# Kernel tuning notes

Hardware: AMD Instinct MI355X
Metric: run time of the kernel (lower is better)

Reference implementation:

```python
import jax, jax.numpy as jnp
import numpy as np

B, T, E, H = 2, 1024, 2048, 32
D = E // H
GROUP = (0.25, 0.25, 0.25, 0.25)
NEG = float(np.finfo(np.float32).min)


def quant_per_token(t, n_bits):
    # smoothquant-style: clamp(absmax, 1e-5) / qmax, per last-dim row
    qmax = 2 ** (n_bits - 1) - 1
    s = jnp.clip(jnp.abs(t).max(-1, keepdims=True), 1e-5, None) / qmax
    return jnp.round(t / s) * s


def w8a8_linear(x, W, b, quant_out=False):
    xq = quant_per_token(x, 8)           # per-token act quant
    Wq = quant_per_token(W, 8)           # per-output-channel weight quant (W: [out, in])
    y = xq @ Wq.T + b
    return quant_per_token(y, 8) if quant_out else y


def to_heads(x):
    # [B, T, E] -> [B*H, T, D]
    return x.reshape(B, T, H, D).transpose(0, 2, 1, 3).reshape(B * H, T, D)


def setup_inputs() -> dict:
    key = jax.random.key(0)
    ks = jax.random.split(key, 9)
    hidden_states = jax.random.normal(ks[0], (B, T, E), jnp.float32)
    causal = jnp.where(jnp.tril(jnp.ones((T, T), bool)), 0.0, NEG).astype(jnp.float32)
    attention_mask = jnp.broadcast_to(causal[None, None], (B, 1, T, T))
    w = 0.02
    return {
        'hidden_states': hidden_states,
        'attention_mask': attention_mask,
        'Wq': jax.random.normal(ks[1], (E, E), jnp.float32) * w,
        'bq': jax.random.normal(ks[2], (E,), jnp.float32) * w,
        'Wk': jax.random.normal(ks[3], (E, E), jnp.float32) * w,
        'bk': jax.random.normal(ks[4], (E,), jnp.float32) * w,
        'Wv': jax.random.normal(ks[5], (E, E), jnp.float32) * w,
        'bv': jax.random.normal(ks[6], (E,), jnp.float32) * w,
        'Wo': jax.random.normal(ks[7], (E, E), jnp.float32) * w,
        'bo': jax.random.normal(ks[8], (E,), jnp.float32) * w,
    }


def reference(hidden_states, attention_mask, Wq, bq, Wk, bk, Wv, bv, Wo, bo):
    scaling = D ** -0.5
    q = w8a8_linear(hidden_states, Wq, bq, quant_out=True) * scaling  # [B,T,E]
    k = w8a8_linear(hidden_states, Wk, bk)                            # [B,T,E]
    v = w8a8_linear(hidden_states, Wv, bv)                            # [B,T,E]

    # ---- heavy-hitter scoring pass (pre-4bit-quant K) ----
    q1, k1 = to_heads(q), to_heads(k)                                 # [BH,T,D]
    aw = jnp.einsum('btd,bsd->bts', q1, k1)                           # [BH,T,T]
    aw = aw.reshape(B, H, T, T) + attention_mask
    aw = jnp.maximum(aw, NEG).reshape(B * H, T, T)
    tmp_attn = jax.nn.softmax(aw, axis=-1)
    acc = tmp_attn.sum(axis=1).sum(axis=0)[None, :]                   # [1,T]
    row_vector = jnp.arange(T, 0, -1).astype(jnp.float32)[None, :]    # T, T-1, ..., 1
    acc = acc / row_vector / (B * H)

    # ---- group-wise top-k heavy-hitter selection ----
    range_size_or = int(T / len(GROUP) / 2)
    start = 1
    idx_list = []
    for i, ratio in enumerate(GROUP):
        rs = int(T * ratio)
        end = min(start + rs - 1, T) if i < len(GROUP) - 1 else T
        partial = acc[:, start - 1:end]
        _, ti = jax.lax.top_k(partial, range_size_or)
        idx_list.append(ti + start - 1)
        start = end + 1
    topk_idx = jnp.concatenate(idx_list, axis=-1).reshape(-1)

    # ---- mixed-precision K quantization ----
    k_abs = jnp.abs(k)
    # fake_quant_mix (8-bit): amax(...)[0] in torch indexes batch 0 -> scales [T,1]
    s_mix = jnp.clip(k_abs.max(-1, keepdims=True)[0] / 127.0, 1e-5, None)  # [T,1]
    k_imp = jnp.round(k / s_mix) * s_mix
    # fake_quant (4-bit, per-row): clamp then divide by 7
    s4 = jnp.clip(k_abs.max(-1, keepdims=True), 1e-5, None) / 7.0
    kq = jnp.round(k / s4) * s4
    kq = kq.at[:, topk_idx, :].set(k_imp[:, topk_idx, :])
    # fake_quant_v (4-bit, per-tensor)
    sv = jnp.clip(jnp.abs(v).max(), 1e-5, None) / 7.0
    vq = jnp.round(v / sv) * sv

    # ---- actual attention with quantized K/V ----
    q2, k2, v2 = to_heads(q), to_heads(kq), to_heads(vq)
    aw2 = jnp.einsum('btd,bsd->bts', q2, k2).reshape(B, H, T, T) + attention_mask
    aw2 = jnp.maximum(aw2, NEG).reshape(B * H, T, T)
    probs = jax.nn.softmax(aw2, axis=-1)
    out = jnp.einsum('bts,bsd->btd', probs, v2)                       # [BH,T,D]
    out = out.reshape(B, H, T, D).transpose(0, 2, 1, 3).reshape(B, T, E)
    return w8a8_linear(out, Wo, bo)
```

## Files before the change

### kernel.cpp

```cpp
#include <hip/hip_runtime.h>
#include <stdint.h>

#define NEG_INF (-__builtin_inff())
#define L2E 1.4426950408889634f

namespace {
constexpr int kT   = 1024;
constexpr int kE   = 2048;
}

using bf16x8 = __attribute__((ext_vector_type(8))) short;
using f32x4  = __attribute__((ext_vector_type(4))) float;
using i32x4  = __attribute__((ext_vector_type(4))) int;

#define MFMA_BF16(a, b, c) __builtin_amdgcn_mfma_f32_16x16x32_bf16((a), (b), (c), 0, 0, 0)
#define MFMA_I8(a, b, c)   __builtin_amdgcn_mfma_i32_16x16x64_i8((a), (b), (c), 0, 0, 0)

__device__ __forceinline__ void gload16(const void* g, void* l) {
  __builtin_amdgcn_global_load_lds((const __attribute__((address_space(1))) unsigned*)g,
                                   (__attribute__((address_space(3))) unsigned*)l, 16, 0, 0);
}
__device__ __forceinline__ unsigned bfr(float x) {
  unsigned u = __float_as_uint(x);
  return (u + 0x7FFFu + ((u >> 16) & 1u)) >> 16;
}
__device__ __forceinline__ float bf2f(unsigned h) { return __uint_as_float(h << 16); }
__device__ __forceinline__ unsigned pk2(float a, float b) { return bfr(a) | (bfr(b) << 16); }
__device__ __forceinline__ float fexp2(float x) { return __builtin_amdgcn_exp2f(x); }

__device__ __forceinline__ float waveReduceMax(float v) {
#pragma unroll
  for (int o = 32; o > 0; o >>= 1) v = fmaxf(v, __shfl_down(v, o, 64));
  return v;
}
__device__ __forceinline__ float waveReduceSum(float v) {
#pragma unroll
  for (int o = 32; o > 0; o >>= 1) v += __shfl_down(v, o, 64);
  return v;
}
__device__ __forceinline__ float blockMax256(float v, float* r4) {
  const int tid = threadIdx.x;
  float wm = waveReduceMax(v);
  if ((tid & 63) == 0) r4[tid >> 6] = wm;
  __syncthreads();
  float bm = fmaxf(fmaxf(r4[0], r4[1]), fmaxf(r4[2], r4[3]));
  __syncthreads();
  return bm;
}

__global__ __launch_bounds__(256) void k_rowquant_i8(const float* __restrict__ X,
                                                     int8_t* __restrict__ Xq,
                                                     float* __restrict__ S) {
  const int row = blockIdx.x;
  const int tid = threadIdx.x;
  const float* x = X + (size_t)row * kE;
  __shared__ float r4[4];
  float am = 0.f;
#pragma unroll
  for (int it = 0; it < 2; ++it) {
    const float4 v = *reinterpret_cast<const float4*>(x + (size_t)(it * 256 + tid) * 4);
    am = fmaxf(am, fmaxf(fmaxf(fabsf(v.x), fabsf(v.y)), fmaxf(fabsf(v.z), fabsf(v.w))));
  }
  const float bm = blockMax256(am, r4);
  const float s = fmaxf(bm, 1e-5f) / 127.f;
  int8_t* xq = Xq + (size_t)row * kE;
#pragma unroll
  for (int it = 0; it < 2; ++it) {
    const int i = (it * 256 + tid) * 4;
    const float4 v = *reinterpret_cast<const float4*>(x + i);
    char4 q;
    q.x = (char)(int)rintf(v.x / s);
    q.y = (char)(int)rintf(v.y / s);
    q.z = (char)(int)rintf(v.z / s);
    q.w = (char)(int)rintf(v.w / s);
    *reinterpret_cast<char4*>(xq + i) = q;
  }
  if (tid == 0) S[row] = s;
}

__global__ __launch_bounds__(256) void k_rowquant_w4(const float* __restrict__ W0,
                                                     const float* __restrict__ W1,
                                                     const float* __restrict__ W2,
                                                     const float* __restrict__ W3,
                                                     int8_t* __restrict__ Q0,
                                                     int8_t* __restrict__ Q1,
                                                     int8_t* __restrict__ Q2,
                                                     int8_t* __restrict__ Q3,
                                                     float* __restrict__ S) {
  const int y = blockIdx.y;
  const float* W = (y == 0) ? W0 : (y == 1) ? W1 : (y == 2) ? W2 : W3;
  int8_t* Qp = (y == 0) ? Q0 : (y == 1) ? Q1 : (y == 2) ? Q2 : Q3;
  const int row = blockIdx.x;
  const int tid = threadIdx.x;
  const float* x = W + (size_t)row * kE;
  __shared__ float r4[4];
  float am = 0.f;
#pragma unroll
  for (int it = 0; it < 2; ++it) {
    const float4 v = *reinterpret_cast<const float4*>(x + (size_t)(it * 256 + tid) * 4);
    am = fmaxf(am, fmaxf(fmaxf(fabsf(v.x), fabsf(v.y)), fmaxf(fabsf(v.z), fabsf(v.w))));
  }
  const float bm = blockMax256(am, r4);
  const float s = fmaxf(bm, 1e-5f) / 127.f;
  int8_t* xq = Qp + (size_t)row * kE;
#pragma unroll
  for (int it = 0; it < 2; ++it) {
    const int i = (it * 256 + tid) * 4;
    const float4 v = *reinterpret_cast<const float4*>(x + i);
    char4 q;
    q.x = (char)(int)rintf(v.x / s);
    q.y = (char)(int)rintf(v.y / s);
    q.z = (char)(int)rintf(v.z / s);
    q.w = (char)(int)rintf(v.w / s);
    *reinterpret_cast<char4*>(xq + i) = q;
  }
  if (tid == 0) S[y * kE + row] = s;
}

__global__ __launch_bounds__(256) void k_q2int(const float* __restrict__ Qb,
                                               short* __restrict__ qi,
                                               float* __restrict__ sqg) {
  const int row = blockIdx.x;
  const int tid = threadIdx.x;
  const float* x = Qb + (size_t)row * kE;
  __shared__ float r4[4];
  float am = 0.f;
  float4 v[2];
#pragma unroll
  for (int it = 0; it < 2; ++it) {
    v[it] = *reinterpret_cast<const float4*>(x + (size_t)(it * 256 + tid) * 4);
    am = fmaxf(am, fmaxf(fmaxf(fabsf(v[it].x), fabsf(v[it].y)), fmaxf(fabsf(v[it].z), fabsf(v[it].w))));
  }
  const float bm = blockMax256(am, r4);
  const float s = fmaxf(bm, 1e-5f) / 127.f;
#pragma unroll
  for (int it = 0; it < 2; ++it) {
    const int i = (it * 256 + tid) * 4;
    short4 q;
    q.x = (short)bfr(rintf(v[it].x / s));
    q.y = (short)bfr(rintf(v[it].y / s));
    q.z = (short)bfr(rintf(v[it].z / s));
    q.w = (short)bfr(rintf(v[it].w / s));
    *reinterpret_cast<short4*>(qi + (size_t)row * kE + i) = q;
  }
  if (tid == 0) sqg[row] = s * 0.125f;
}

__global__ __launch_bounds__(256) void k_ksplitscale(const float* __restrict__ Kb,
                                                     short* __restrict__ khi,
                                                     short* __restrict__ klo,
                                                     float* __restrict__ s4,
                                                     float* __restrict__ smix) {
  const int row = blockIdx.x;
  const int tid = threadIdx.x;
  const float* x = Kb + (size_t)row * kE;
  __shared__ float r4[4];
  float am = 0.f;
  float4 v[2];
#pragma unroll
  for (int it = 0; it < 2; ++it) {
    v[it] = *reinterpret_cast<const float4*>(x + (size_t)(it * 256 + tid) * 4);
    am = fmaxf(am, fmaxf(fmaxf(fabsf(v[it].x), fabsf(v[it].y)), fmaxf(fabsf(v[it].z), fabsf(v[it].w))));
  }
  const float bm = blockMax256(am, r4);
#pragma unroll
  for (int it = 0; it < 2; ++it) {
    const int i = (it * 256 + tid) * 4;
    short4 hh, ll;
    unsigned hb;
    hb = bfr(v[it].x); hh.x = (short)hb; ll.x = (short)bfr(v[it].x - bf2f(hb));
    hb = bfr(v[it].y); hh.y = (short)hb; ll.y = (short)bfr(v[it].y - bf2f(hb));
    hb = bfr(v[it].z); hh.z = (short)hb; ll.z = (short)bfr(v[it].z - bf2f(hb));
    hb = bfr(v[it].w); hh.w = (short)hb; ll.w = (short)bfr(v[it].w - bf2f(hb));
    *reinterpret_cast<short4*>(khi + (size_t)row * kE + i) = hh;
    *reinterpret_cast<short4*>(klo + (size_t)row * kE + i) = ll;
  }
  if (tid == 0) {
    s4[row] = fmaxf(bm, 1e-5f) / 7.f;
    if (row < kT) smix[row] = fmaxf(bm / 127.f, 1e-5f);
  }
}

__global__ void k_init(unsigned* vmax) {
  if (threadIdx.x == 0 && blockIdx.x == 0) *vmax = 0u;
}

__global__ __launch_bounds__(256) void k_vabsmax(const float* __restrict__ Vb,
                                                 unsigned* __restrict__ vmax) {
  const int row = blockIdx.x;
  const int tid = threadIdx.x;
  const float* x = Vb + (size_t)row * kE;
  __shared__ float r4[4];
  float am = 0.f;
#pragma unroll
  for (int it = 0; it < 2; ++it) {
    const float4 v = *reinterpret_cast<const float4*>(x + (size_t)(it * 256 + tid) * 4);
    am = fmaxf(am, fmaxf(fmaxf(fabsf(v.x), fabsf(v.y)), fmaxf(fabsf(v.z), fabsf(v.w))));
  }
  const float bm = blockMax256(am, r4);
  if (tid == 0) atomicMax(vmax, __float_as_uint(bm));
}

__global__ __launch_bounds__(256) void k_kint(const float* __restrict__ Kb,
                                              const float* __restrict__ s4,
                                              const float* __restrict__ smix,
                                              const int* __restrict__ sel,
                                              short* __restrict__ ki,
                                              float* __restrict__ skg) {
  const int row = blockIdx.x;
  const int tid = threadIdx.x;
  const int t = row & (kT - 1);
  const float s = sel[t] ? smix[t] : s4[row];
  const float* x = Kb + (size_t)row * kE;
#pragma unroll
  for (int it = 0; it < 2; ++it) {
    const int i = (it * 256 + tid) * 4;
    const float4 v = *reinterpret_cast<const float4*>(x + i);
    short4 q;
    q.x = (short)bfr(rintf(v.x / s));
    q.y = (short)bfr(rintf(v.y / s));
    q.z = (short)bfr(rintf(v.z / s));
    q.w = (short)bfr(rintf(v.w / s));
    *reinterpret_cast<short4*>(ki + (size_t)row * kE + i) = q;
  }
  if (tid == 0) skg[row] = s;
}

__global__ __launch_bounds__(256) void k_vint(const float* __restrict__ Vb,
                                              const unsigned* __restrict__ vmax,
                                              short* __restrict__ vt) {
  const int tt = blockIdx.x;
  const int bh = blockIdx.y;
  const int b = bh >> 5, h = bh & 31;
  const float sv = fmaxf(__uint_as_float(*vmax), 1e-5f) / 7.f;
  __shared__ short tr[64][80];
  const int tid = threadIdx.x;
#pragma unroll
  for (int i = 0; i < 4; ++i) {
    const int e = i * 256 + tid;
    const int tok = e >> 4, d4 = (e & 15) * 4;
    const float4 v = *reinterpret_cast<const float4*>(
        &Vb[(size_t)(b * kT + tt * 64 + tok) * kE + h * 64 + d4]);
    tr[d4 + 0][tok] = (short)bfr(rintf(v.x / sv));
    tr[d4 + 1][tok] = (short)bfr(rintf(v.y / sv));
    tr[d4 + 2][tok] = (short)bfr(rintf(v.z / sv));
    tr[d4 + 3][tok] = (short)bfr(rintf(v.w / sv));
  }
  __syncthreads();
#pragma unroll
  for (int i = 0; i < 2; ++i) {
    const int e = i * 256 + tid;
    const int d = e >> 3, u = e & 7;
    const bf16x8 row = *reinterpret_cast<const bf16x8*>(&tr[d][u * 8]);
    *reinterpret_cast<bf16x8*>(&vt[(size_t)(bh * 64 + d) * kT + tt * 64 + u * 8]) = row;
  }
}

__device__ __forceinline__ void gemm_i8_body(const int8_t* __restrict__ A,
                                             const float* __restrict__ sa,
                                             const int8_t* __restrict__ Bw,
                                             const float* __restrict__ sw,
                                             const float* __restrict__ bias,
                                             float* __restrict__ Y,
                                             int8_t* As0, int8_t* As1,
                                             int8_t* Bs0, int8_t* Bs1) {
  int8_t* Asb[2] = {As0, As1};
  int8_t* Bsb[2] = {Bs0, Bs1};
  const int tid = threadIdx.x;
  const int lane = tid & 63, w = tid >> 6;
  const int g = lane >> 4, c16 = lane & 15;
  const int m0 = blockIdx.y * 128, n0 = blockIdx.x * 128;
  const int wm = (w >> 1) * 64, wn = (w & 1) * 64;

  const i32x4 zero = {0, 0, 0, 0};
  i32x4 acc[4][4];
#pragma unroll
  for (int i = 0; i < 4; ++i)
#pragma unroll
    for (int j = 0; j < 4; ++j) acc[i][j] = zero;

  const int srow = tid >> 2, su = tid & 3;
  auto stage = [&](int buf, int k0) {
#pragma unroll
    for (int i = 0; i < 2; ++i) {
      const int row = i * 64 + srow;
      const int uoff = ((su ^ (row & 3)) << 4);
      gload16(A + (size_t)(m0 + row) * kE + k0 + uoff, &Asb[buf][row * 64 + su * 16]);
      gload16(Bw + (size_t)(n0 + row) * kE + k0 + uoff, &Bsb[buf][row * 64 + su * 16]);
    }
  };

  stage(0, 0);
  __syncthreads();
  int cur = 0;
  for (int k0 = 0; k0 < kE; k0 += 64) {
    if (k0 + 64 < kE) stage(cur ^ 1, k0 + 64);
    i32x4 av[4], bv[4];
#pragma unroll
    for (int f = 0; f < 4; ++f) {
      const int ar = wm + f * 16 + c16;
      av[f] = *reinterpret_cast<const i32x4*>(&Asb[cur][ar * 64 + ((g ^ (c16 & 3)) << 4)]);
      const int br = wn + f * 16 + c16;
      bv[f] = *reinterpret_cast<const i32x4*>(&Bsb[cur][br * 64 + ((g ^ (c16 & 3)) << 4)]);
    }
#pragma unroll
    for (int fm = 0; fm < 4; ++fm)
#pragma unroll
      for (int fn = 0; fn < 4; ++fn) acc[fm][fn] = MFMA_I8(av[fm], bv[fn], acc[fm][fn]);
    __syncthreads();
    cur ^= 1;
  }

#pragma unroll
  for (int fn = 0; fn < 4; ++fn) {
    const int n = n0 + wn + fn * 16 + c16;
    const float swn = sw[n], bn = bias[n];
#pragma unroll
    for (int fm = 0; fm < 4; ++fm) {
#pragma unroll
      for (int r = 0; r < 4; ++r) {
        const int m = m0 + wm + fm * 16 + g * 4 + r;
        Y[(size_t)m * kE + n] = (float)acc[fm][fn][r] * sa[m] * swn + bn;
      }
    }
  }
}

__global__ __launch_bounds__(256) void k_gemm_i8(const int8_t* __restrict__ A,
                                                 const float* __restrict__ sa,
                                                 const int8_t* __restrict__ Bw,
                                                 const float* __restrict__ sw,
                                                 const float* __restrict__ bias,
                                                 float* __restrict__ Y) {
  __shared__ int8_t As[2][128 * 64];
  __shared__ int8_t Bs[2][128 * 64];
  gemm_i8_body(A, sa, Bw, sw, bias, Y, As[0], As[1], Bs[0], Bs[1]);
}

__global__ __launch_bounds__(256) void k_gemm_qkv(const int8_t* __restrict__ A,
                                                  const float* __restrict__ sa,
                                                  const int8_t* __restrict__ Wq,
                                                  const int8_t* __restrict__ Wk,
                                                  const int8_t* __restrict__ Wv,
                                                  const float* __restrict__ sWall,
                                                  const float* __restrict__ bq,
                                                  const float* __restrict__ bk,
                                                  const float* __restrict__ bv,
                                                  float* __restrict__ qb,
                                                  float* __restrict__ kb,
                                                  float* __restrict__ vb) {
  __shared__ int8_t As[2][128 * 64];
  __shared__ int8_t Bs[2][128 * 64];
  const int z = blockIdx.z;
  const int8_t* Bw = (z == 0) ? Wq : (z == 1) ? Wk : Wv;
  const float* sw = sWall + (size_t)z * kE;
  const float* bias = (z == 0) ? bq : (z == 1) ? bk : bv;
  float* Y = (z == 0) ? qb : (z == 1) ? kb : vb;
  gemm_i8_body(A, sa, Bw, sw, bias, Y, As[0], As[1], Bs[0], Bs[1]);
}

__global__ __launch_bounds__(256) void k_attn1(const short* __restrict__ qi,
                                               const short* __restrict__ khi,
                                               const short* __restrict__ klo,
                                               const float* __restrict__ sqg,
                                               float* __restrict__ accPart) {
  const int r1 = blockIdx.x, r2 = 15 - r1, bh = blockIdx.y;
  const int b = bh >> 5, h = bh & 31;
  const int tid = threadIdx.x, lane = tid & 63, w = tid >> 6;
  const int g = lane >> 4, c16 = lane & 15;
  const int swz = c16 & 7;

  __shared__ short qs1[64 * 64];
  __shared__ short qs2[64 * 64];
  __shared__ short hbuf[2][64 * 64];
  __shared__ short lbuf[2][64 * 64];
  __shared__ float accL[1024];
  __shared__ float Arow[128], Crow[128];

  for (int i = tid; i < 1024; i += 256) accL[i] = 0.f;

  const int st8 = tid >> 3, su = tid & 7;
  {
    const int tokb1 = b * kT + r1 * 64;
    const int tokb2 = b * kT + r2 * 64;
#pragma unroll
    for (int i = 0; i < 2; ++i) {
      const int tok = i * 32 + st8;
      const int co = ((su ^ (tok & 7)) << 3);
      gload16(qi + (size_t)(tokb1 + tok) * kE + h * 64 + co, &qs1[tok * 64 + su * 8]);
      gload16(qi + (size_t)(tokb2 + tok) * kE + h * 64 + co, &qs2[tok * 64 + su * 8]);
    }
  }
  auto stage = [&](int buf, int kt) {
    const int tokb = b * kT + kt * 64;
#pragma unroll
    for (int i = 0; i < 2; ++i) {
      const int tok = i * 32 + st8;
      const size_t gsrc = (size_t)(tokb + tok) * kE + h * 64 + ((su ^ (tok & 7)) << 3);
      gload16(khi + gsrc, &hbuf[buf][tok * 64 + su * 8]);
      gload16(klo + gsrc, &lbuf[buf][tok * 64 + su * 8]);
    }
  };

  stage(0, 0);
  __syncthreads();

  const int qrow = w * 16 + c16;
  const bf16x8 q1_0 = *reinterpret_cast<const bf16x8*>(&qs1[qrow * 64 + ((g ^ swz) << 3)]);
  const bf16x8 q1_1 = *reinterpret_cast<const bf16x8*>(&qs1[qrow * 64 + (((4 + g) ^ swz) << 3)]);
  const bf16x8 q2_0 = *reinterpret_cast<const bf16x8*>(&qs2[qrow * 64 + ((g ^ swz) << 3)]);
  const bf16x8 q2_1 = *reinterpret_cast<const bf16x8*>(&qs2[qrow * 64 + (((4 + g) ^ swz) << 3)]);
  const float A1c = sqg[b * kT + r1 * 64 + qrow] * L2E;
  const float A2c = sqg[b * kT + r2 * 64 + qrow] * L2E;

  float m1 = NEG_INF, l1 = 0.f, m2_ = NEG_INF, l2 = 0.f;
  int cur = 0;

  for (int kt = 0; kt <= r2; ++kt) {
    if (kt < r2) stage(cur ^ 1, kt + 1);
    const bool act1 = kt <= r1;
    float p1[4][4], p2[4][4];
    float pm1 = NEG_INF, pm2 = NEG_INF;
#pragma unroll
    for (int f = 0; f < 4; ++f) {
      const int tokl = f * 16 + c16;
      const bf16x8 ah0 = *reinterpret_cast<const bf16x8*>(&hbuf[cur][tokl * 64 + ((g ^ swz) << 3)]);
      const bf16x8 ah1 = *reinterpret_cast<const bf16x8*>(&hbuf[cur][tokl * 64 + (((4 + g) ^ swz) << 3)]);
      const bf16x8 al0 = *reinterpret_cast<const bf16x8*>(&lbuf[cur][tokl * 64 + ((g ^ swz) << 3)]);
      const bf16x8 al1 = *reinterpret_cast<const bf16x8*>(&lbuf[cur][tokl * 64 + (((4 + g) ^ swz) << 3)]);
      f32x4 sB = {0.f, 0.f, 0.f, 0.f};
      sB = MFMA_BF16(ah0, q2_0, sB);
      sB = MFMA_BF16(ah1, q2_1, sB);
      sB = MFMA_BF16(al0, q2_0, sB);
      sB = MFMA_BF16(al1, q2_1, sB);
      f32x4 sA = {0.f, 0.f, 0.f, 0.f};
      if (act1) {
        sA = MFMA_BF16(ah0, q1_0, sA);
        sA = MFMA_BF16(ah1, q1_1, sA);
        sA = MFMA_BF16(al0, q1_0, sA);
        sA = MFMA_BF16(al1, q1_1, sA);
      }
#pragma unroll
      for (int r = 0; r < 4; ++r) {
        const int tokd = f * 16 + g * 4 + r;
        float s2 = sB[r] * A2c;
        if (kt == r2 && tokd > qrow) s2 = NEG_INF;
        p2[f][r] = s2;
        pm2 = fmaxf(pm2, s2);
        float s1 = sA[r] * A1c;
        if (kt == r1 && tokd > qrow) s1 = NEG_INF;
        p1[f][r] = s1;
        pm1 = fmaxf(pm1, s1);
      }
    }
    {
      pm2 = fmaxf(pm2, __shfl_xor(pm2, 16));
      pm2 = fmaxf(pm2, __shfl_xor(pm2, 32));
      const bool upd = pm2 > m2_ + 8.f;
      const float mn = upd ? fmaxf(m2_, pm2) : m2_;
      const float fsc = fexp2(m2_ - mn);
      float rs = 0.f;
#pragma unroll
      for (int f = 0; f < 4; ++f)
#pragma unroll
        for (int r = 0; r < 4; ++r) rs += fexp2(p2[f][r] - mn);
      rs += __shfl_xor(rs, 16);
      rs += __shfl_xor(rs, 32);
      l2 = l2 * fsc + rs;
      m2_ = mn;
    }
    if (act1) {
      pm1 = fmaxf(pm1, __shfl_xor(pm1, 16));
      pm1 = fmaxf(pm1, __shfl_xor(pm1, 32));
      const bool upd = pm1 > m1 + 8.f;
      const float mn = upd ? fmaxf(m1, pm1) : m1;
      const float fsc = fexp2(m1 - mn);
      float rs = 0.f;
#pragma unroll
      for (int f = 0; f < 4; ++f)
#pragma unroll
        for (int r = 0; r < 4; ++r) rs += fexp2(p1[f][r] - mn);
      rs += __shfl_xor(rs, 16);
      rs += __shfl_xor(rs, 32);
      l1 = l1 * fsc + rs;
      m1 = mn;
    }
    __syncthreads();
    cur ^= 1;
  }

  if (g == 0) {
    Arow[qrow] = A1c;
    Crow[qrow] = -(m1 + __builtin_amdgcn_logf(l1));
    Arow[64 + qrow] = A2c;
    Crow[64 + qrow] = -(m2_ + __builtin_amdgcn_logf(l2));
  }
  stage(0, 0);
  __syncthreads();

  bf16x8 qa1_0[4], qa1_1[4], qa2_0[4], qa2_1[4];
  float Ar1[4][4], Cr1[4][4], Ar2[4][4], Cr2[4][4];
#pragma unroll
  for (int f = 0; f < 4; ++f) {
    const int qr = f * 16 + c16;
    qa1_0[f] = *reinterpret_cast<const bf16x8*>(&qs1[qr * 64 + ((g ^ swz) << 3)]);
    qa1_1[f] = *reinterpret_cast<const bf16x8*>(&qs1[qr * 64 + (((4 + g) ^ swz) << 3)]);
    qa2_0[f] = *reinterpret_cast<const bf16x8*>(&qs2[qr * 64 + ((g ^ swz) << 3)]);
    qa2_1[f] = *reinterpret_cast<const bf16x8*>(&qs2[qr * 64 + (((4 + g) ^ swz) << 3)]);
#pragma unroll
    for (int r = 0; r < 4; ++r) {
      const int tokd = f * 16 + g * 4 + r;
      Ar1[f][r] = Arow[tokd];
      Cr1[f][r] = Crow[tokd];
      Ar2[f][r] = Arow[64 + tokd];
      Cr2[f][r] = Crow[64 + tokd];
    }
  }

  const int ktokL = w * 16 + c16;
  cur = 0;
  for (int kt = 0; kt <= r2; ++kt) {
    if (kt < r2) stage(cur ^ 1, kt + 1);
    const bf16x8 kh0 = *reinterpret_cast<const bf16x8*>(&hbuf[cur][ktokL * 64 + ((g ^ swz) << 3)]);
    const bf16x8 kh1 = *reinterpret_cast<const bf16x8*>(&hbuf[cur][ktokL * 64 + (((4 + g) ^ swz) << 3)]);
    const bf16x8 kl0 = *reinterpret_cast<const bf16x8*>(&lbuf[cur][ktokL * 64 + ((g ^ swz) << 3)]);
    const bf16x8 kl1 = *reinterpret_cast<const bf16x8*>(&lbuf[cur][ktokL * 64 + (((4 + g) ^ swz) << 3)]);
    float csum = 0.f;
    if (kt < r2) {
#pragma unroll
      for (int f = 0; f < 4; ++f) {
        f32x4 sf = {0.f, 0.f, 0.f, 0.f};
        sf = MFMA_BF16(qa2_0[f], kh0, sf);
        sf = MFMA_BF16(qa2_1[f], kh1, sf);
        sf = MFMA_BF16(qa2_0[f], kl0, sf);
        sf = MFMA_BF16(qa2_1[f], kl1, sf);
#pragma unroll
        for (int r = 0; r < 4; ++r) csum += fexp2(fmaf(sf[r], Ar2[f][r], Cr2[f][r]));
      }
    } else {
#pragma unroll
      for (int f = 0; f < 4; ++f) {
        f32x4 sf = {0.f, 0.f, 0.f, 0.f};
        sf = MFMA_BF16(qa2_0[f], kh0, sf);
        sf = MFMA_BF16(qa2_1[f], kh1, sf);
        sf = MFMA_BF16(qa2_0[f], kl0, sf);
        sf = MFMA_BF16(qa2_1[f], kl1, sf);
#pragma unroll
        for (int r = 0; r < 4; ++r) {
          const float v = fexp2(fmaf(sf[r], Ar2[f][r], Cr2[f][r]));
          if (ktokL <= (f * 16 + g * 4 + r)) csum += v;
        }
      }
    }
    if (kt <= r1) {
      if (kt < r1) {
#pragma unroll
        for (int f = 0; f < 4; ++f) {
          f32x4 sf = {0.f, 0.f, 0.f, 0.f};
          sf = MFMA_BF16(qa1_0[f], kh0, sf);
          sf = MFMA_BF16(qa1_1[f], kh1, sf);
          sf = MFMA_BF16(qa1_0[f], kl0, sf);
          sf = MFMA_BF16(qa1_1[f], kl1, sf);
#pragma unroll
          for (int r = 0; r < 4; ++r) csum += fexp2(fmaf(sf[r], Ar1[f][r], Cr1[f][r]));
        }
      } else {
#pragma unroll
        for (int f = 0; f < 4; ++f) {
          f32x4 sf = {0.f, 0.f, 0.f, 0.f};
          sf = MFMA_BF16(qa1_0[f], kh0, sf);
          sf = MFMA_BF16(qa1_1[f], kh1, sf);
          sf = MFMA_BF16(qa1_0[f], kl0, sf);
          sf = MFMA_BF16(qa1_1[f], kl1, sf);
#pragma unroll
          for (int r = 0; r < 4; ++r) {
            const float v = fexp2(fmaf(sf[r], Ar1[f][r], Cr1[f][r]));
            if (ktokL <= (f * 16 + g * 4 + r)) csum += v;
          }
        }
      }
    }
    csum += __shfl_xor(csum, 16);
    csum += __shfl_xor(csum, 32);
    if (g == 0) accL[kt * 64 + ktokL] += csum;
    __syncthreads();
    cur ^= 1;
  }

  for (int i = tid; i < 1024; i += 256)
    accPart[(size_t)(bh * 8 + r1) * 1024 + i] = accL[i];
}

__global__ __launch_bounds__(256) void k_accreduce(const float* __restrict__ part,
                                                   float* __restrict__ acc) {
  const int j = blockIdx.x;
  const int tid = threadIdx.x;
  float s = 0.f;
  for (int p = tid; p < 512; p += 256) s += part[(size_t)p * 1024 + j];
  __shared__ float r4[4];
  const float ws = waveReduceSum(s);
  if ((tid & 63) == 0) r4[tid >> 6] = ws;
  __syncthreads();
  if (tid == 0) {
    const float t = r4[0] + r4[1] + r4[2] + r4[3];
    acc[j] = t / (float)(kT - j) / 64.f;
  }
}

__global__ __launch_bounds__(256) void k_topk(const float* __restrict__ acc,
                                              int* __restrict__ sel) {
  const int gq = blockIdx.x;
  const int i = threadIdx.x;
  __shared__ float v[256];
  const float vi = acc[gq * 256 + i];
  v[i] = vi;
  __syncthreads();
  int rank = 0;
  for (int j = 0; j < 256; ++j) {
    const float vj = v[j];
    rank += (vj > vi) || (vj == vi && j < i);
  }
  sel[gq * 256 + i] = (rank < 128) ? 1 : 0;
}

__global__ __launch_bounds__(256) void k_attn2(const short* __restrict__ qi,
                                               const short* __restrict__ ki,
                                               const short* __restrict__ vt,
                                               const float* __restrict__ sqg,
                                               const float* __restrict__ skg,
                                               const unsigned* __restrict__ vmax,
                                               float* __restrict__ ctx) {
  const int r1 = blockIdx.x, r2 = 15 - r1, bh = blockIdx.y;
  const int b = bh >> 5, h = bh & 31;
  const int tid = threadIdx.x, lane = tid & 63, w = tid >> 6;
  const int g = lane >> 4, c16 = lane & 15;
  const int swz = c16 & 7;
  const int wrow = w * 16 + c16;

  __shared__ short kbuf[2][64 * 64];
  __shared__ short vbuf[2][64 * 64];
  __shared__ float skl[2][64];

  const int qtokA = b * kT + r1 * 64 + wrow;
  const int qtokB = b * kT + r2 * 64 + wrow;
  bf16x8 qfA[2], qfB[2];
  qfA[0] = *reinterpret_cast<const bf16x8*>(qi + (size_t)qtokA * kE + h * 64 + g * 8);
  qfA[1] = *reinterpret_cast<const bf16x8*>(qi + (size_t)qtokA * kE + h * 64 + 32 + g * 8);
  qfB[0] = *reinterpret_cast<const bf16x8*>(qi + (size_t)qtokB * kE + h * 64 + g * 8);
  qfB[1] = *reinterpret_cast<const bf16x8*>(qi + (size_t)qtokB * kE + h * 64 + 32 + g * 8);
  const float sqA = sqg[qtokA] * L2E;
  const float sqB = sqg[qtokB] * L2E;
  const float sv = fmaxf(__uint_as_float(*vmax), 1e-5f) / 7.f;

  const int st8 = tid >> 3, su = tid & 7;
  auto stage = [&](int buf, int kt) {
    const int tokb = b * kT + kt * 64;
#pragma unroll
    for (int i = 0; i < 2; ++i) {
      const int tok = i * 32 + st8;
      gload16(ki + (size_t)(tokb + tok) * kE + h * 64 + ((su ^ (tok & 7)) << 3),
              &kbuf[buf][tok * 64 + su * 8]);
      gload16(vt + (size_t)(bh * 64 + tok) * kT + kt * 64 + ((su ^ (tok & 7)) << 3),
              &vbuf[buf][tok * 64 + su * 8]);
    }
    if (tid < 64) skl[buf][tid] = skg[tokb + tid];
  };

  float mA = NEG_INF, lA = 0.f, mB = NEG_INF, lB = 0.f;
  f32x4 otA[4], otB[4];
#pragma unroll
  for (int f = 0; f < 4; ++f) {
    otA[f] = (f32x4){0.f, 0.f, 0.f, 0.f};
    otB[f] = (f32x4){0.f, 0.f, 0.f, 0.f};
  }

  stage(0, 0);
  __syncthreads();
  int cur = 0;

  const int srcLo = c16 | ((g & 1) << 5);
  const int srcHi = srcLo | 16;
  const bool selq = ((g >> 1) & 1) != 0;

  for (int kt = 0; kt <= r2; ++kt) {
    if (kt < r2) stage(cur ^ 1, kt + 1);
    const bool act1 = kt <= r1;

    f32x4 sfB4[4], sfA4[4];
#pragma unroll
    for (int f = 0; f < 4; ++f) {
      const int tokl = f * 16 + c16;
      const bf16x8 k0 = *reinterpret_cast<const bf16x8*>(&kbuf[cur][tokl * 64 + ((g ^ swz) << 3)]);
      const bf16x8 k1 = *reinterpret_cast<const bf16x8*>(&kbuf[cur][tokl * 64 + (((4 + g) ^ swz) << 3)]);
      f32x4 s = {0.f, 0.f, 0.f, 0.f};
      s = MFMA_BF16(k0, qfB[0], s);
      s = MFMA_BF16(k1, qfB[1], s);
      sfB4[f] = s;
      f32x4 sa = {0.f, 0.f, 0.f, 0.f};
      if (act1) {
        sa = MFMA_BF16(k0, qfA[0], sa);
        sa = MFMA_BF16(k1, qfA[1], sa);
      }
      sfA4[f] = sa;
    }

    {
      float p[4][4];
      float pm = NEG_INF;
#pragma unroll
      for (int f = 0; f < 4; ++f)
#pragma unroll
        for (int r = 0; r < 4; ++r) {
          const int tokd = f * 16 + g * 4 + r;
          float s2 = sfB4[f][r] * skl[cur][tokd] * sqB;
          if (kt == r2 && tokd > wrow) s2 = NEG_INF;
          p[f][r] = s2;
          pm = fmaxf(pm, s2);
        }
      pm = fmaxf(pm, __shfl_xor(pm, 16));
      pm = fmaxf(pm, __shfl_xor(pm, 32));
      const bool upd = pm > mB + 8.f;
      const float mn = upd ? fmaxf(mB, pm) : mB;
      const float fsc = fexp2(mB - mn);
      mB = mn;
      float rs = 0.f;
#pragma unroll
      for (int f = 0; f < 4; ++f)
#pragma unroll
        for (int r = 0; r < 4; ++r) {
          const float e = fexp2(p[f][r] - mn);
          p[f][r] = e;
          rs += e;
        }
      rs += __shfl_xor(rs, 16);
      rs += __shfl_xor(rs, 32);
      lB = lB * fsc + rs;
      if (__any(upd)) {
#pragma unroll
        for (int f = 0; f < 4; ++f)
#pragma unroll
          for (int r = 0; r < 4; ++r) otB[f][r] *= fsc;
      }
#pragma unroll
      for (int c = 0; c < 2; ++c) {
        const unsigned q0a = pk2(p[2 * c][0], p[2 * c][1]);
        const unsigned q0b = pk2(p[2 * c][2], p[2 * c][3]);
        const unsigned q1a = pk2(p[2 * c + 1][0], p[2 * c + 1][1]);
        const unsigned q1b = pk2(p[2 * c + 1][2], p[2 * c + 1][3]);
        unsigned a0, a1;
        union { unsigned u[4]; bf16x8 v; } Bh;
        a0 = __shfl(q0a, srcLo); a1 = __shfl(q1a, srcLo); Bh.u[0] = selq ? a1 : a0;
        a0 = __shfl(q0b, srcLo); a1 = __shfl(q1b, srcLo); Bh.u[1] = selq ? a1 : a0;
        a0 = __shfl(q0a, srcHi); a1 = __shfl(q1a, srcHi); Bh.u[2] = selq ? a1 : a0;
        a0 = __shfl(q0b, srcHi); a1 = __shfl(q1b, srcHi); Bh.u[3] = selq ? a1 : a0;
#pragma unroll
        for (int fd = 0; fd < 4; ++fd) {
          const int d = fd * 16 + c16;
          const bf16x8 va = *reinterpret_cast<const bf16x8*>(
              &vbuf[cur][d * 64 + ((((c << 2) | g) ^ swz) << 3)]);
          otB[fd] = MFMA_BF16(va, Bh.v, otB[fd]);
        }
      }
    }

    if (act1) {
      float p[4][4];
      float pm = NEG_INF;
#pragma unroll
      for (int f = 0; f < 4; ++f)
#pragma unroll
        for (int r = 0; r < 4; ++r) {
          const int tokd = f * 16 + g * 4 + r;
          float s2 = sfA4[f][r] * skl[cur][tokd] * sqA;
          if (kt == r1 && tokd > wrow) s2 = NEG_INF;
          p[f][r] = s2;
          pm = fmaxf(pm, s2);
        }
      pm = fmaxf(pm, __shfl_xor(pm, 16));
      pm = fmaxf(pm, __shfl_xor(pm, 32));
      const bool upd = pm > mA + 8.f;
      const float mn = upd ? fmaxf(mA, pm) : mA;
      const float fsc = fexp2(mA - mn);
      mA = mn;
      float rs = 0.f;
#pragma unroll
      for (int f = 0; f < 4; ++f)
#pragma unroll
        for (int r = 0; r < 4; ++r) {
          const float e = fexp2(p[f][r] - mn);
          p[f][r] = e;
          rs += e;
        }
      rs += __shfl_xor(rs, 16);
      rs += __shfl_xor(rs, 32);
      lA = lA * fsc + rs;
      if (__any(upd)) {
#pragma unroll
        for (int f = 0; f < 4; ++f)
#pragma unroll
          for (int r = 0; r < 4; ++r) otA[f][r] *= fsc;
      }
#pragma unroll
      for (int c = 0; c < 2; ++c) {
        const unsigned q0a = pk2(p[2 * c][0], p[2 * c][1]);
        const unsigned q0b = pk2(p[2 * c][2], p[2 * c][3]);
        const unsigned q1a = pk2(p[2 * c + 1][0], p[2 * c + 1][1]);
        const unsigned q1b = pk2(p[2 * c + 1][2], p[2 * c + 1][3]);
        unsigned a0, a1;
        union { unsigned u[4]; bf16x8 v; } Bh;
        a0 = __shfl(q0a, srcLo); a1 = __shfl(q1a, srcLo); Bh.u[0] = selq ? a1 : a0;
        a0 = __shfl(q0b, srcLo); a1 = __shfl(q1b, srcLo); Bh.u[1] = selq ? a1 : a0;
        a0 = __shfl(q0a, srcHi); a1 = __shfl(q1a, srcHi); Bh.u[2] = selq ? a1 : a0;
        a0 = __shfl(q0b, srcHi); a1 = __shfl(q1b, srcHi); Bh.u[3] = selq ? a1 : a0;
#pragma unroll
        for (int fd = 0; fd < 4; ++fd) {
          const int d = fd * 16 + c16;
          const bf16x8 va = *reinterpret_cast<const bf16x8*>(
              &vbuf[cur][d * 64 + ((((c << 2) | g) ^ swz) << 3)]);
          otA[fd] = MFMA_BF16(va, Bh.v, otA[fd]);
        }
      }
    }

    __syncthreads();
    cur ^= 1;
  }

  const float ilA = sv / lA;
  const float ilB = sv / lB;
#pragma unroll
  for (int fd = 0; fd < 4; ++fd) {
    float4 oA, oB;
    oA.x = otA[fd][0] * ilA; oA.y = otA[fd][1] * ilA;
    oA.z = otA[fd][2] * ilA; oA.w = otA[fd][3] * ilA;
    oB.x = otB[fd][0] * ilB; oB.y = otB[fd][1] * ilB;
    oB.z = otB[fd][2] * ilB; oB.w = otB[fd][3] * ilB;
    *reinterpret_cast<float4*>(&ctx[(size_t)qtokA * kE + h * 64 + fd * 16 + g * 4]) = oA;
    *reinterpret_cast<float4*>(&ctx[(size_t)qtokB * kE + h * 64 + fd * 16 + g * 4]) = oB;
  }
}

extern "C" void kernel_launch(void* const* d_in, const int* in_sizes, int n_in,
                              void* d_out, int out_size, void* d_ws, size_t ws_size,
                              hipStream_t stream) {
  (void)in_sizes; (void)n_in; (void)out_size; (void)ws_size;
  const float* hs = (const float*)d_in[0];
  const float* Wq = (const float*)d_in[2];
  const float* bq = (const float*)d_in[3];
  const float* Wk = (const float*)d_in[4];
  const float* bk = (const float*)d_in[5];
  const float* Wv = (const float*)d_in[6];
  const float* bv = (const float*)d_in[7];
  const float* Wo = (const float*)d_in[8];
  const float* bo = (const float*)d_in[9];
  float* out = (float*)d_out;

  char* p = (char*)d_ws;
  auto take = [&](size_t bytes) {
    char* r = p;
    p += (bytes + 255) & ~(size_t)255;
    return r;
  };
  float* qb  = (float*)take((size_t)2048 * 2048 * 4);
  float* kb  = (float*)take((size_t)2048 * 2048 * 4);
  float* vb  = (float*)take((size_t)2048 * 2048 * 4);
  float* ctx = (float*)take((size_t)2048 * 2048 * 4);
  short* qiB = (short*)take((size_t)2048 * 2048 * 2);
  int8_t* xq  = (int8_t*)take((size_t)2048 * 2048);
  int8_t* woq = (int8_t*)take((size_t)2048 * 2048);
  float* sX    = (float*)take(2048 * 4);
  float* sWall = (float*)take(4 * 2048 * 4);
  float* sC    = (float*)take(2048 * 4);
  float* s4v   = (float*)take(2048 * 4);
  float* smix  = (float*)take(1024 * 4);
  float* accv  = (float*)take(1024 * 4);
  int*   sel   = (int*)take(1024 * 4);
  float* sqg   = (float*)take(2048 * 4);
  float* skg   = (float*)take(2048 * 4);
  unsigned* vmax = (unsigned*)take(256);

  short* khi = (short*)qb;
  short* klo = (short*)qb + (size_t)2048 * 2048;
  short* kint = khi;
  short* vtp  = klo;
  float* accPart = ctx;
  int8_t* wqq = (int8_t*)ctx + ((size_t)2 << 20);
  int8_t* wkq = (int8_t*)ctx + ((size_t)6 << 20);
  int8_t* wvq = (int8_t*)ctx + ((size_t)10 << 20);
  int8_t* cq = xq;

  k_rowquant_i8<<<2048, 256, 0, stream>>>(hs, xq, sX);
  k_rowquant_w4<<<dim3(2048, 4), 256, 0, stream>>>(Wq, Wk, Wv, Wo, wqq, wkq, wvq, woq, sWall);

  k_gemm_qkv<<<dim3(16, 16, 3), 256, 0, stream>>>(xq, sX, wqq, wkq, wvq, sWall,
                                                  bq, bk, bv, qb, kb, vb);

  k_q2int<<<2048, 256, 0, stream>>>(qb, qiB, sqg);
  k_ksplitscale<<<2048, 256, 0, stream>>>(kb, khi, klo, s4v, smix);
  k_init<<<1, 64, 0, stream>>>(vmax);
  k_vabsmax<<<2048, 256, 0, stream>>>(vb, vmax);

  k_attn1<<<dim3(8, 64), 256, 0, stream>>>(qiB, khi, klo, sqg, accPart);
  k_accreduce<<<1024, 256, 0, stream>>>(accPart, accv);
  k_topk<<<4, 256, 0, stream>>>(accv, sel);

  k_kint<<<2048, 256, 0, stream>>>(kb, s4v, smix, sel, kint, skg);
  k_vint<<<dim3(16, 64), 256, 0, stream>>>(vb, vmax, vtp);

  k_attn2<<<dim3(8, 64), 256, 0, stream>>>(qiB, kint, vtp, sqg, skg, vmax, ctx);

  k_rowquant_i8<<<2048, 256, 0, stream>>>(ctx, cq, sC);
  k_gemm_i8<<<dim3(16, 16), 256, 0, stream>>>(cq, sC, woq, sWall + 3 * 2048, bo, out);
}
```

Measured before the change: 254.7 us.

## Fuse quant/prep kernels, remap GEMM block order and change LDS swizzle

```diff
diff --git a/kernel.cpp b/kernel.cpp
--- a/kernel.cpp
+++ b/kernel.cpp
@@ -48,6 +48,53 @@
   return bm;
 }
 
+__global__ __launch_bounds__(256) void k_rowquant_all(const float* __restrict__ Xh,
+                                                      const float* __restrict__ W0,
+                                                      const float* __restrict__ W1,
+                                                      const float* __restrict__ W2,
+                                                      const float* __restrict__ W3,
+                                                      int8_t* __restrict__ Qh,
+                                                      int8_t* __restrict__ Q0,
+                                                      int8_t* __restrict__ Q1,
+                                                      int8_t* __restrict__ Q2,
+                                                      int8_t* __restrict__ Q3,
+                                                      float* __restrict__ sX,
+                                                      float* __restrict__ sWall,
+                                                      unsigned* __restrict__ vmax) {
+  const int y = blockIdx.y;
+  const float* X = (y == 0) ? Xh : (y == 1) ? W0 : (y == 2) ? W1 : (y == 3) ? W2 : W3;
+  int8_t* Qp = (y == 0) ? Qh : (y == 1) ? Q0 : (y == 2) ? Q1 : (y == 3) ? Q2 : Q3;
+  const int row = blockIdx.x;
+  const int tid = threadIdx.x;
+  if (row == 0 && y == 0 && tid == 0) *vmax = 0u;
+  const float* x = X + (size_t)row * kE;
+  __shared__ float r4[4];
+  float am = 0.f;
+  float4 v[2];
+#pragma unroll
+  for (int it = 0; it < 2; ++it) {
+    v[it] = *reinterpret_cast<const float4*>(x + (size_t)(it * 256 + tid) * 4);
+    am = fmaxf(am, fmaxf(fmaxf(fabsf(v[it].x), fabsf(v[it].y)), fmaxf(fabsf(v[it].z), fabsf(v[it].w))));
+  }
+  const float bm = blockMax256(am, r4);
+  const float s = fmaxf(bm, 1e-5f) / 127.f;
+  int8_t* xq = Qp + (size_t)row * kE;
+#pragma unroll
+  for (int it = 0; it < 2; ++it) {
+    const int i = (it * 256 + tid) * 4;
+    char4 q;
+    q.x = (char)(int)rintf(v[it].x / s);
+    q.y = (char)(int)rintf(v[it].y / s);
+    q.z = (char)(int)rintf(v[it].z / s);
+    q.w = (char)(int)rintf(v[it].w / s);
+    *reinterpret_cast<char4*>(xq + i) = q;
+  }
+  if (tid == 0) {
+    if (y == 0) sX[row] = s;
+    else sWall[(y - 1) * kE + row] = s;
+  }
+}
+
 __global__ __launch_bounds__(256) void k_rowquant_i8(const float* __restrict__ X,
                                                      int8_t* __restrict__ Xq,
                                                      float* __restrict__ S) {
@@ -56,10 +103,11 @@
   const float* x = X + (size_t)row * kE;
   __shared__ float r4[4];
   float am = 0.f;
+  float4 v[2];
 #pragma unroll
   for (int it = 0; it < 2; ++it) {
-    const float4 v = *reinterpret_cast<const float4*>(x + (size_t)(it * 256 + tid) * 4);
-    am = fmaxf(am, fmaxf(fmaxf(fabsf(v.x), fabsf(v.y)), fmaxf(fabsf(v.z), fabsf(v.w))));
+    v[it] = *reinterpret_cast<const float4*>(x + (size_t)(it * 256 + tid) * 4);
+    am = fmaxf(am, fmaxf(fmaxf(fabsf(v[it].x), fabsf(v[it].y)), fmaxf(fabsf(v[it].z), fabsf(v[it].w))));
   }
   const float bm = blockMax256(am, r4);
   const float s = fmaxf(bm, 1e-5f) / 127.f;
@@ -67,138 +115,93 @@
 #pragma unroll
   for (int it = 0; it < 2; ++it) {
     const int i = (it * 256 + tid) * 4;
-    const float4 v = *reinterpret_cast<const float4*>(x + i);
     char4 q;
-    q.x = (char)(int)rintf(v.x / s);
-    q.y = (char)(int)rintf(v.y / s);
-    q.z = (char)(int)rintf(v.z / s);
-    q.w = (char)(int)rintf(v.w / s);
+    q.x = (char)(int)rintf(v[it].x / s);
+    q.y = (char)(int)rintf(v[it].y / s);
+    q.z = (char)(int)rintf(v[it].z / s);
+    q.w = (char)(int)rintf(v[it].w / s);
     *reinterpret_cast<char4*>(xq + i) = q;
   }
   if (tid == 0) S[row] = s;
 }
 
-__global__ __launch_bounds__(256) void k_rowquant_w4(const float* __restrict__ W0,
-                                                     const float* __restrict__ W1,
-                                                     const float* __restrict__ W2,
-                                                     const float* __restrict__ W3,
-                                                     int8_t* __restrict__ Q0,
-                                                     int8_t* __restrict__ Q1,
-                                                     int8_t* __restrict__ Q2,
-                                                     int8_t* __restrict__ Q3,
-                                                     float* __restrict__ S) {
-  const int y = blockIdx.y;
-  const float* W = (y == 0) ? W0 : (y == 1) ? W1 : (y == 2) ? W2 : W3;
-  int8_t* Qp = (y == 0) ? Q0 : (y == 1) ? Q1 : (y == 2) ? Q2 : Q3;
+__global__ __launch_bounds__(256) void k_prep(const float* __restrict__ Qb,
+                                              const float* __restrict__ Kb,
+                                              const float* __restrict__ Vb,
+                                              short* __restrict__ qi,
+                                              float* __restrict__ sqg,
+                                              short* __restrict__ khi,
+                                              short* __restrict__ klo,
+                                              float* __restrict__ s4,
+                                              float* __restrict__ smix,
+                                              unsigned* __restrict__ vmax) {
   const int row = blockIdx.x;
   const int tid = threadIdx.x;
-  const float* x = W + (size_t)row * kE;
   __shared__ float r4[4];
-  float am = 0.f;
-#pragma unroll
-  for (int it = 0; it < 2; ++it) {
-    const float4 v = *reinterpret_cast<const float4*>(x + (size_t)(it * 256 + tid) * 4);
-    am = fmaxf(am, fmaxf(fmaxf(fabsf(v.x), fabsf(v.y)), fmaxf(fabsf(v.z), fabsf(v.w))));
-  }
-  const float bm = blockMax256(am, r4);
-  const float s = fmaxf(bm, 1e-5f) / 127.f;
-  int8_t* xq = Qp + (size_t)row * kE;
-#pragma unroll
-  for (int it = 0; it < 2; ++it) {
-    const int i = (it * 256 + tid) * 4;
-    const float4 v = *reinterpret_cast<const float4*>(x + i);
-    char4 q;
-    q.x = (char)(int)rintf(v.x / s);
-    q.y = (char)(int)rintf(v.y / s);
-    q.z = (char)(int)rintf(v.z / s);
-    q.w = (char)(int)rintf(v.w / s);
-    *reinterpret_cast<char4*>(xq + i) = q;
-  }
-  if (tid == 0) S[y * kE + row] = s;
-}
-
-__global__ __launch_bounds__(256) void k_q2int(const float* __restrict__ Qb,
-                                               short* __restrict__ qi,
-                                               float* __restrict__ sqg) {
-  const int row = blockIdx.x;
-  const int tid = threadIdx.x;
-  const float* x = Qb + (size_t)row * kE;
-  __shared__ float r4[4];
-  float am = 0.f;
-  float4 v[2];
-#pragma unroll
-  for (int it = 0; it < 2; ++it) {
-    v[it] = *reinterpret_cast<const float4*>(x + (size_t)(it * 256 + tid) * 4);
-    am = fmaxf(am, fmaxf(fmaxf(fabsf(v[it].x), fabsf(v[it].y)), fmaxf(fabsf(v[it].z), fabsf(v[it].w))));
-  }
-  const float bm = blockMax256(am, r4);
-  const float s = fmaxf(bm, 1e-5f) / 127.f;
-#pragma unroll
-  for (int it = 0; it < 2; ++it) {
-    const int i = (it * 256 + tid) * 4;
-    short4 q;
-    q.x = (short)bfr(rintf(v[it].x / s));
-    q.y = (short)bfr(rintf(v[it].y / s));
-    q.z = (short)bfr(rintf(v[it].z / s));
-    q.w = (short)bfr(rintf(v[it].w / s));
-    *reinterpret_cast<short4*>(qi + (size_t)row * kE + i) = q;
-  }
-  if (tid == 0) sqg[row] = s * 0.125f;
-}
-
-__global__ __launch_bounds__(256) void k_ksplitscale(const float* __restrict__ Kb,
-                                                     short* __restrict__ khi,
-                                                     short* __restrict__ klo,
-                                                     float* __restrict__ s4,
-                                                     float* __restrict__ smix) {
-  const int row = blockIdx.x;
-  const int tid = threadIdx.x;
-  const float* x = Kb + (size_t)row * kE;
-  __shared__ float r4[4];
-  float am = 0.f;
-  float4 v[2];
-#pragma unroll
-  for (int it = 0; it < 2; ++it) {
-    v[it] = *reinterpret_cast<const float4*>(x + (size_t)(it * 256 + tid) * 4);
-    am = fmaxf(am, fmaxf(fmaxf(fabsf(v[it].x), fabsf(v[it].y)), fmaxf(fabsf(v[it].z), fabsf(v[it].w))));
-  }
-  const float bm = blockMax256(am, r4);
-#pragma unroll
-  for (int it = 0; it < 2; ++it) {
-    const int i = (it * 256 + tid) * 4;
-    short4 hh, ll;
-    unsigned hb;
-    hb = bfr(v[it].x); hh.x = (short)hb; ll.x = (short)bfr(v[it].x - bf2f(hb));
-    hb = bfr(v[it].y); hh.y = (short)hb; ll.y = (short)bfr(v[it].y - bf2f(hb));
-    hb = bfr(v[it].z); hh.z = (short)hb; ll.z = (short)bfr(v[it].z - bf2f(hb));
-    hb = bfr(v[it].w); hh.w = (short)hb; ll.w = (short)bfr(v[it].w - bf2f(hb));
-    *reinterpret_cast<short4*>(khi + (size_t)row * kE + i) = hh;
-    *reinterpret_cast<short4*>(klo + (size_t)row * kE + i) = ll;
-  }
-  if (tid == 0) {
-    s4[row] = fmaxf(bm, 1e-5f) / 7.f;
-    if (row < kT) smix[row] = fmaxf(bm / 127.f, 1e-5f);
-  }
-}
-
-__global__ void k_init(unsigned* vmax) {
-  if (threadIdx.x == 0 && blockIdx.x == 0) *vmax = 0u;
-}
-
-__global__ __launch_bounds__(256) void k_vabsmax(const float* __restrict__ Vb,
-                                                 unsigned* __restrict__ vmax) {
-  const int row = blockIdx.x;
-  const int tid = threadIdx.x;
-  const float* x = Vb + (size_t)row * kE;
-  __shared__ float r4[4];
-  float am = 0.f;
-#pragma unroll
-  for (int it = 0; it < 2; ++it) {
-    const float4 v = *reinterpret_cast<const float4*>(x + (size_t)(it * 256 + tid) * 4);
-    am = fmaxf(am, fmaxf(fmaxf(fabsf(v.x), fabsf(v.y)), fmaxf(fabsf(v.z), fabsf(v.w))));
-  }
-  const float bm = blockMax256(am, r4);
-  if (tid == 0) atomicMax(vmax, __float_as_uint(bm));
+
+  {
+    const float* x = Qb + (size_t)row * kE;
+    float am = 0.f;
+    float4 v[2];
+#pragma unroll
+    for (int it = 0; it < 2; ++it) {
+      v[it] = *reinterpret_cast<const float4*>(x + (size_t)(it * 256 + tid) * 4);
+      am = fmaxf(am, fmaxf(fmaxf(fabsf(v[it].x), fabsf(v[it].y)), fmaxf(fabsf(v[it].z), fabsf(v[it].w))));
+    }
+    const float bm = blockMax256(am, r4);
+    const float s = fmaxf(bm, 1e-5f) / 127.f;
+#pragma unroll
+    for (int it = 0; it < 2; ++it) {
+      const int i = (it * 256 + tid) * 4;
+      short4 q;
+      q.x = (short)bfr(rintf(v[it].x / s));
+      q.y = (short)bfr(rintf(v[it].y / s));
+      q.z = (short)bfr(rintf(v[it].z / s));
+      q.w = (short)bfr(rintf(v[it].w / s));
+      *reinterpret_cast<short4*>(qi + (size_t)row * kE + i) = q;
+    }
+    if (tid == 0) sqg[row] = s * 0.125f;
+  }
+
+  {
+    const float* x = Kb + (size_t)row * kE;
+    float am = 0.f;
+    float4 v[2];
+#pragma unroll
+    for (int it = 0; it < 2; ++it) {
+      v[it] = *reinterpret_cast<const float4*>(x + (size_t)(it * 256 + tid) * 4);
+      am = fmaxf(am, fmaxf(fmaxf(fabsf(v[it].x), fabsf(v[it].y)), fmaxf(fabsf(v[it].z), fabsf(v[it].w))));
+    }
+    const float bm = blockMax256(am, r4);
+#pragma unroll
+    for (int it = 0; it < 2; ++it) {
+      const int i = (it * 256 + tid) * 4;
+      short4 hh, ll;
+      unsigned hb;
+      hb = bfr(v[it].x); hh.x = (short)hb; ll.x = (short)bfr(v[it].x - bf2f(hb));
+      hb = bfr(v[it].y); hh.y = (short)hb; ll.y = (short)bfr(v[it].y - bf2f(hb));
+      hb = bfr(v[it].z); hh.z = (short)hb; ll.z = (short)bfr(v[it].z - bf2f(hb));
+      hb = bfr(v[it].w); hh.w = (short)hb; ll.w = (short)bfr(v[it].w - bf2f(hb));
+      *reinterpret_cast<short4*>(khi + (size_t)row * kE + i) = hh;
+      *reinterpret_cast<short4*>(klo + (size_t)row * kE + i) = ll;
+    }
+    if (tid == 0) {
+      s4[row] = fmaxf(bm, 1e-5f) / 7.f;
+      if (row < kT) smix[row] = fmaxf(bm / 127.f, 1e-5f);
+    }
+  }
+
+  {
+    const float* x = Vb + (size_t)row * kE;
+    float am = 0.f;
+#pragma unroll
+    for (int it = 0; it < 2; ++it) {
+      const float4 v = *reinterpret_cast<const float4*>(x + (size_t)(it * 256 + tid) * 4);
+      am = fmaxf(am, fmaxf(fmaxf(fabsf(v.x), fabsf(v.y)), fmaxf(fabsf(v.z), fabsf(v.w))));
+    }
+    const float bm = blockMax256(am, r4);
+    if (tid == 0) atomicMax(vmax, __float_as_uint(bm));
+  }
 }
 
 __global__ __launch_bounds__(256) void k_kint(const float* __restrict__ Kb,
@@ -256,7 +259,8 @@
   }
 }
 
-__device__ __forceinline__ void gemm_i8_body(const int8_t* __restrict__ A,
+__device__ __forceinline__ void gemm_i8_body(int m0, int n0,
+                                             const int8_t* __restrict__ A,
                                              const float* __restrict__ sa,
                                              const int8_t* __restrict__ Bw,
                                              const float* __restrict__ sw,
@@ -269,8 +273,8 @@
   const int tid = threadIdx.x;
   const int lane = tid & 63, w = tid >> 6;
   const int g = lane >> 4, c16 = lane & 15;
-  const int m0 = blockIdx.y * 128, n0 = blockIdx.x * 128;
   const int wm = (w >> 1) * 64, wn = (w & 1) * 64;
+  const int rsw = (c16 >> 1) & 3;
 
   const i32x4 zero = {0, 0, 0, 0};
   i32x4 acc[4][4];
@@ -280,11 +284,12 @@
     for (int j = 0; j < 4; ++j) acc[i][j] = zero;
 
   const int srow = tid >> 2, su = tid & 3;
+  const int ssw = (srow >> 1) & 3;
   auto stage = [&](int buf, int k0) {
 #pragma unroll
     for (int i = 0; i < 2; ++i) {
       const int row = i * 64 + srow;
-      const int uoff = ((su ^ (row & 3)) << 4);
+      const int uoff = ((su ^ ssw) << 4);
       gload16(A + (size_t)(m0 + row) * kE + k0 + uoff, &Asb[buf][row * 64 + su * 16]);
       gload16(Bw + (size_t)(n0 + row) * kE + k0 + uoff, &Bsb[buf][row * 64 + su * 16]);
     }
@@ -299,9 +304,9 @@
 #pragma unroll
     for (int f = 0; f < 4; ++f) {
       const int ar = wm + f * 16 + c16;
-      av[f] = *reinterpret_cast<const i32x4*>(&Asb[cur][ar * 64 + ((g ^ (c16 & 3)) << 4)]);
+      av[f] = *reinterpret_cast<const i32x4*>(&Asb[cur][ar * 64 + ((g ^ rsw) << 4)]);
       const int br = wn + f * 16 + c16;
-      bv[f] = *reinterpret_cast<const i32x4*>(&Bsb[cur][br * 64 + ((g ^ (c16 & 3)) << 4)]);
+      bv[f] = *reinterpret_cast<const i32x4*>(&Bsb[cur][br * 64 + ((g ^ rsw) << 4)]);
     }
 #pragma unroll
     for (int fm = 0; fm < 4; ++fm)
@@ -334,7 +339,10 @@
                                                  float* __restrict__ Y) {
   __shared__ int8_t As[2][128 * 64];
   __shared__ int8_t Bs[2][128 * 64];
-  gemm_i8_body(A, sa, Bw, sw, bias, Y, As[0], As[1], Bs[0], Bs[1]);
+  const int linear = blockIdx.x + (blockIdx.y << 4);
+  const int nid = (linear & 7) * 32 + (linear >> 3);
+  const int x = nid & 15, y = nid >> 4;
+  gemm_i8_body(y * 128, x * 128, A, sa, Bw, sw, bias, Y, As[0], As[1], Bs[0], Bs[1]);
 }
 
 __global__ __launch_bounds__(256) void k_gemm_qkv(const int8_t* __restrict__ A,
@@ -351,12 +359,14 @@
                                                   float* __restrict__ vb) {
   __shared__ int8_t As[2][128 * 64];
   __shared__ int8_t Bs[2][128 * 64];
-  const int z = blockIdx.z;
+  const int linear = blockIdx.x + (blockIdx.y << 4) + (blockIdx.z << 8);
+  const int nid = (linear & 7) * 96 + (linear >> 3);
+  const int x = nid & 15, y = (nid >> 4) & 15, z = nid >> 8;
   const int8_t* Bw = (z == 0) ? Wq : (z == 1) ? Wk : Wv;
   const float* sw = sWall + (size_t)z * kE;
   const float* bias = (z == 0) ? bq : (z == 1) ? bk : bv;
   float* Y = (z == 0) ? qb : (z == 1) ? kb : vb;
-  gemm_i8_body(A, sa, Bw, sw, bias, Y, As[0], As[1], Bs[0], Bs[1]);
+  gemm_i8_body(y * 128, x * 128, A, sa, Bw, sw, bias, Y, As[0], As[1], Bs[0], Bs[1]);
 }
 
 __global__ __launch_bounds__(256) void k_attn1(const short* __restrict__ qi,
@@ -889,16 +899,14 @@
   int8_t* wvq = (int8_t*)ctx + ((size_t)10 << 20);
   int8_t* cq = xq;
 
-  k_rowquant_i8<<<2048, 256, 0, stream>>>(hs, xq, sX);
-  k_rowquant_w4<<<dim3(2048, 4), 256, 0, stream>>>(Wq, Wk, Wv, Wo, wqq, wkq, wvq, woq, sWall);
+  k_rowquant_all<<<dim3(2048, 5), 256, 0, stream>>>(hs, Wq, Wk, Wv, Wo,
+                                                    xq, wqq, wkq, wvq, woq,
+                                                    sX, sWall, vmax);
 
   k_gemm_qkv<<<dim3(16, 16, 3), 256, 0, stream>>>(xq, sX, wqq, wkq, wvq, sWall,
                                                   bq, bk, bv, qb, kb, vb);
 
-  k_q2int<<<2048, 256, 0, stream>>>(qb, qiB, sqg);
-  k_ksplitscale<<<2048, 256, 0, stream>>>(kb, khi, klo, s4v, smix);
-  k_init<<<1, 64, 0, stream>>>(vmax);
-  k_vabsmax<<<2048, 256, 0, stream>>>(vb, vmax);
+  k_prep<<<2048, 256, 0, stream>>>(qb, kb, vb, qiB, sqg, khi, klo, s4v, smix, vmax);
 
   k_attn1<<<dim3(8, 64), 256, 0, stream>>>(qiB, khi, klo, sqg, accPart);
   k_accreduce<<<1024, 256, 0, stream>>>(accPart, accv);
```

New measurement: 232.6 us. -8.7%, faster.
